# Optimization experiments

Hardware: AMD Instinct MI355X
Metric: run time of the kernel (lower is better)

The kernel has to match this reference:

```python
import jax, jax.numpy as jnp
import numpy as np

NUM_PITCHES = 128
RHYTHM_DIM = 10
HARMONY_DIM = 12
VOCAB_SIZE = 390
EPS = 1e-08


def setup_inputs() -> dict:
    key = jax.random.key(0)
    k_tok, k_w1, k_w2 = jax.random.split(key, 3)
    B, T = 1024, 8192
    stats_dim = NUM_PITCHES + RHYTHM_DIM + HARMONY_DIM  # 150
    midi_tokens = jax.random.randint(k_tok, (B, T), 0, VOCAB_SIZE, dtype=jnp.int64 if jax.config.jax_enable_x64 else jnp.int32)
    W1 = jax.random.normal(k_w1, (stats_dim, 256), dtype=jnp.float32) * 0.05
    b1 = jnp.zeros((256,), dtype=jnp.float32)
    W2 = jax.random.normal(k_w2, (256, 128), dtype=jnp.float32) * 0.05
    b2 = jnp.zeros((128,), dtype=jnp.float32)
    return {"midi_tokens": midi_tokens, "W1": W1, "b1": b1, "W2": W2, "b2": b2}


def _compute_stats(midi_tokens):
    """Vectorized pitch histogram + rhythm + harmony stats. midi_tokens: (B, T) int."""
    B, T = midi_tokens.shape
    # Pitch distribution: histogram of tokens % 128 per batch row, via one flat scatter-add.
    pitch = midi_tokens % NUM_PITCHES  # (B, T) in [0, 128)
    flat_bins = (jnp.arange(B, dtype=pitch.dtype)[:, None] * NUM_PITCHES + pitch).reshape(-1)
    hist = jnp.zeros((B * NUM_PITCHES,), dtype=jnp.float32).at[flat_bins].add(1.0)
    pitch_dist = hist.reshape(B, NUM_PITCHES)
    pitch_dist = pitch_dist / (pitch_dist.sum(axis=-1, keepdims=True) + EPS)
    # Rhythm: mean and (unbiased, torch-default) std; remaining 8 dims are zeros.
    tf = midi_tokens.astype(jnp.float32)
    mean = tf.mean(axis=-1)
    std = jnp.sqrt(((tf - mean[:, None]) ** 2).sum(axis=-1) / (T - 1))
    rhythm = jnp.zeros((B, RHYTHM_DIM), dtype=jnp.float32)
    rhythm = rhythm.at[:, 0].set(mean).at[:, 1].set(std)
    # Harmony: original uses torch.rand(12) per row; deterministic uniform here.
    harmony = jax.random.uniform(jax.random.key(42), (B, HARMONY_DIM), dtype=jnp.float32)
    return jnp.concatenate([pitch_dist, rhythm, harmony], axis=-1)  # (B, 150)


def reference(midi_tokens, W1, b1, W2, b2):
    stats = _compute_stats(midi_tokens)
    h = jax.nn.relu(stats @ W1 + b1)
    return h @ W2 + b2  # (B, feature_dim=128)
```

## Files before the change

kernel.cpp:

```cpp
#include <hip/hip_runtime.h>
#include <stdint.h>
#include <math.h>

#define T_SEQ 8192

typedef int vint4 __attribute__((ext_vector_type(4)));

__device__ __forceinline__ uint32_t rotl32(uint32_t x, int n) {
    return (x << n) | (x >> (32 - n));
}

__device__ uint32_t jax_threefry_bits_12288(uint32_t idx) {
    const uint32_t k0 = 0u, k1 = 42u, k2 = 0u ^ 42u ^ 0x1BD11BDAu;
    uint32_t i = (idx < 6144u) ? idx : (idx - 6144u);
    uint32_t x0 = i + k0;
    uint32_t x1 = (i + 6144u) + k1;
#define TF_R4(a,b,c,d) \
    x0 += x1; x1 = rotl32(x1, a); x1 ^= x0; \
    x0 += x1; x1 = rotl32(x1, b); x1 ^= x0; \
    x0 += x1; x1 = rotl32(x1, c); x1 ^= x0; \
    x0 += x1; x1 = rotl32(x1, d); x1 ^= x0;
    TF_R4(13, 15, 26, 6);   x0 += k1; x1 += k2 + 1u;
    TF_R4(17, 29, 16, 24);  x0 += k2; x1 += k0 + 2u;
    TF_R4(13, 15, 26, 6);   x0 += k0; x1 += k1 + 3u;
    TF_R4(17, 29, 16, 24);  x0 += k1; x1 += k2 + 4u;
    TF_R4(13, 15, 26, 6);   x0 += k2; x1 += k0 + 5u;
#undef TF_R4
    return (idx < 6144u) ? x0 : x1;
}

__global__ __launch_bounds__(512) void fused_kernel(const int* __restrict__ tok,
                                                    const float* __restrict__ W1,
                                                    const float* __restrict__ b1,
                                                    const float* __restrict__ W2,
                                                    const float* __restrict__ b2,
                                                    float* __restrict__ out) {
    const int tid = threadIdx.x;
    const int wave = tid >> 6;
    const int hw = tid >> 5;
    const int r0 = blockIdx.x * 2;

    __shared__ int hist[16][128];
    __shared__ int wsum[8];
    __shared__ unsigned wsq[8];
    __shared__ float s[2][150];
    __shared__ float h[2][256];
    __shared__ float part[2][128];

    for (int i = tid; i < 2048; i += 512) ((int*)hist)[i] = 0;
    __syncthreads();

    {
        const int row_local = tid >> 8;
        const int t256 = tid & 255;
        const vint4* tp = (const vint4*)(tok + (size_t)(r0 + row_local) * T_SEQ);

        vint4 v[8];
#pragma unroll
        for (int j = 0; j < 8; ++j)
            v[j] = __builtin_nontemporal_load(&tp[j * 256 + t256]);

        int sum = 0;
        unsigned sq = 0;
#pragma unroll
        for (int j = 0; j < 8; ++j) {
            atomicAdd(&hist[hw][v[j].x & 127], 1); sum += v[j].x; sq += (unsigned)__mul24(v[j].x, v[j].x);
            atomicAdd(&hist[hw][v[j].y & 127], 1); sum += v[j].y; sq += (unsigned)__mul24(v[j].y, v[j].y);
            atomicAdd(&hist[hw][v[j].z & 127], 1); sum += v[j].z; sq += (unsigned)__mul24(v[j].z, v[j].z);
            atomicAdd(&hist[hw][v[j].w & 127], 1); sum += v[j].w; sq += (unsigned)__mul24(v[j].w, v[j].w);
        }
#pragma unroll
        for (int off = 32; off > 0; off >>= 1) {
            sum += __shfl_down(sum, off);
            sq  += __shfl_down(sq, off);
        }
        if ((tid & 63) == 0) { wsum[wave] = sum; wsq[wave] = sq; }
    }
    __syncthreads();

    if (tid < 300) {
        const int r = tid >= 150;
        const int k = tid - r * 150;
        const int wb = r * 4;
        const int hb = r * 8;
        float val;
        if (k < 128) {
            int hh = (hist[hb][k] + hist[hb + 1][k]) + (hist[hb + 2][k] + hist[hb + 3][k])
                   + (hist[hb + 4][k] + hist[hb + 5][k]) + (hist[hb + 6][k] + hist[hb + 7][k]);
            val = (float)hh * (1.0f / 8192.0f);
        } else if (k == 128) {
            int ss = wsum[wb] + wsum[wb + 1] + wsum[wb + 2] + wsum[wb + 3];
            val = (float)ss * (1.0f / 8192.0f);
        } else if (k == 129) {
            double ss = (double)(wsum[wb] + wsum[wb + 1] + wsum[wb + 2] + wsum[wb + 3]);
            double qq = (double)wsq[wb] + (double)wsq[wb + 1] + (double)wsq[wb + 2] + (double)wsq[wb + 3];
            val = (float)sqrt((qq - ss * ss / 8192.0) / 8191.0);
        } else if (k < 138) {
            val = 0.0f;
        } else {
            uint32_t bits = jax_threefry_bits_12288((uint32_t)(r0 + r) * 12u + (uint32_t)(k - 138));
            val = __uint_as_float((bits >> 9) | 0x3f800000u) - 1.0f;
        }
        s[r][k] = val;
    }
    __syncthreads();

    {
        const int g = tid >> 8, c = tid & 255;
        float acc = b1[c];
#pragma unroll 5
        for (int k = 0; k < 150; ++k)
            acc = fmaf(s[g][k], W1[k * 256 + c], acc);
        h[g][c] = fmaxf(acc, 0.0f);
    }
    __syncthreads();

    {
        const int half = tid >> 8, g = (tid >> 7) & 1, c = tid & 127;
        const float* hr = h[g];
        const int kb = half * 128;
        float acc = half ? 0.0f : b2[c];
#pragma unroll 8
        for (int k = 0; k < 128; ++k)
            acc = fmaf(hr[kb + k], W2[(kb + k) * 128 + c], acc);
        if (half) part[g][c] = acc;
        __syncthreads();
        if (!half) out[(r0 + g) * 128 + c] = acc + part[g][c];
    }
}

extern "C" void kernel_launch(void* const* d_in, const int* in_sizes, int n_in,
                              void* d_out, int out_size, void* d_ws, size_t ws_size,
                              hipStream_t stream) {
    const int*   tok = (const int*)d_in[0];
    const float* W1  = (const float*)d_in[1];
    const float* b1  = (const float*)d_in[2];
    const float* W2  = (const float*)d_in[3];
    const float* b2  = (const float*)d_in[4];
    float* out = (float*)d_out;

    fused_kernel<<<512, 512, 0, stream>>>(tok, W1, b1, W2, b2, out);
}
```

Before: 98.26 us.

## Process four rows per block and share weight loads across rows in MLP

Each block now handles four rows with 1024 threads instead of two rows with 512. The MLP layers split the K dimension across thread groups, and each weight load is reused for all four rows' accumulators. Partial sums are then reduced through shared memory. This is meant to halve global weight traffic per row and cut the per-row MLP tail, in exchange for fewer blocks (256 on a GPU with many CUs), more shared memory, and an extra reduction sync.

New measurement: 98.42 us. Within noise of the previous version (+0.2%).

```diff
diff --git a/kernel.cpp b/kernel.cpp
--- a/kernel.cpp
+++ b/kernel.cpp
@@ -29,25 +29,26 @@
     return (idx < 6144u) ? x0 : x1;
 }
 
-__global__ __launch_bounds__(512) void fused_kernel(const int* __restrict__ tok,
-                                                    const float* __restrict__ W1,
-                                                    const float* __restrict__ b1,
-                                                    const float* __restrict__ W2,
-                                                    const float* __restrict__ b2,
-                                                    float* __restrict__ out) {
+__global__ __launch_bounds__(1024) void fused_kernel(const int* __restrict__ tok,
+                                                     const float* __restrict__ W1,
+                                                     const float* __restrict__ b1,
+                                                     const float* __restrict__ W2,
+                                                     const float* __restrict__ b2,
+                                                     float* __restrict__ out) {
     const int tid = threadIdx.x;
     const int wave = tid >> 6;
     const int hw = tid >> 5;
-    const int r0 = blockIdx.x * 2;
+    const int r0 = blockIdx.x * 4;
 
-    __shared__ int hist[16][128];
-    __shared__ int wsum[8];
-    __shared__ unsigned wsq[8];
-    __shared__ float s[2][150];
-    __shared__ float h[2][256];
-    __shared__ float part[2][128];
+    __shared__ int hist[32][128];
+    __shared__ int wsum[16];
+    __shared__ unsigned wsq[16];
+    __shared__ float s[4][150];
+    __shared__ float h[4][256];
+    __shared__ float part1[4][4][256];
+    __shared__ float part2[4][4][128];
 
-    for (int i = tid; i < 2048; i += 512) ((int*)hist)[i] = 0;
+    for (int i = tid; i < 4096; i += 1024) ((int*)hist)[i] = 0;
     __syncthreads();
 
     {
@@ -78,8 +79,8 @@
     }
     __syncthreads();
 
-    if (tid < 300) {
-        const int r = tid >= 150;
+    if (tid < 600) {
+        const int r = tid / 150;
         const int k = tid - r * 150;
         const int wb = r * 4;
         const int hb = r * 8;
@@ -106,26 +107,56 @@
     __syncthreads();
 
     {
-        const int g = tid >> 8, c = tid & 255;
-        float acc = b1[c];
-#pragma unroll 5
-        for (int k = 0; k < 150; ++k)
-            acc = fmaf(s[g][k], W1[k * 256 + c], acc);
-        h[g][c] = fmaxf(acc, 0.0f);
+        const int c = tid & 255;
+        const int kq = tid >> 8;
+        const int k0 = kq * 38;
+        const int k1 = (kq == 3) ? 150 : (k0 + 38);
+        float a0 = 0.0f, a1 = 0.0f, a2 = 0.0f, a3 = 0.0f;
+        for (int k = k0; k < k1; ++k) {
+            const float w = W1[k * 256 + c];
+            a0 = fmaf(s[0][k], w, a0);
+            a1 = fmaf(s[1][k], w, a1);
+            a2 = fmaf(s[2][k], w, a2);
+            a3 = fmaf(s[3][k], w, a3);
+        }
+        part1[kq][0][c] = a0;
+        part1[kq][1][c] = a1;
+        part1[kq][2][c] = a2;
+        part1[kq][3][c] = a3;
+    }
+    __syncthreads();
+    {
+        const int c = tid & 255;
+        const int r = tid >> 8;
+        float acc = b1[c] + ((part1[0][r][c] + part1[1][r][c]) + (part1[2][r][c] + part1[3][r][c]));
+        h[r][c] = fmaxf(acc, 0.0f);
     }
     __syncthreads();
 
-    {
-        const int half = tid >> 8, g = (tid >> 7) & 1, c = tid & 127;
-        const float* hr = h[g];
-        const int kb = half * 128;
-        float acc = half ? 0.0f : b2[c];
-#pragma unroll 8
-        for (int k = 0; k < 128; ++k)
-            acc = fmaf(hr[kb + k], W2[(kb + k) * 128 + c], acc);
-        if (half) part[g][c] = acc;
-        __syncthreads();
-        if (!half) out[(r0 + g) * 128 + c] = acc + part[g][c];
+    if (tid < 512) {
+        const int c = tid & 127;
+        const int kq = tid >> 7;
+        const int kb = kq * 64;
+        float a0 = 0.0f, a1 = 0.0f, a2 = 0.0f, a3 = 0.0f;
+#pragma unroll 4
+        for (int k = 0; k < 64; ++k) {
+            const float w = W2[(kb + k) * 128 + c];
+            a0 = fmaf(h[0][kb + k], w, a0);
+            a1 = fmaf(h[1][kb + k], w, a1);
+            a2 = fmaf(h[2][kb + k], w, a2);
+            a3 = fmaf(h[3][kb + k], w, a3);
+        }
+        part2[kq][0][c] = a0;
+        part2[kq][1][c] = a1;
+        part2[kq][2][c] = a2;
+        part2[kq][3][c] = a3;
+    }
+    __syncthreads();
+    if (tid < 512) {
+        const int c = tid & 127;
+        const int r = tid >> 7;
+        out[(size_t)(r0 + r) * 128 + c] =
+            b2[c] + ((part2[0][r][c] + part2[1][r][c]) + (part2[2][r][c] + part2[3][r][c]));
     }
 }
 
@@ -139,5 +170,5 @@
     const float* b2  = (const float*)d_in[4];
     float* out = (float*)d_out;
 
-    fused_kernel<<<512, 512, 0, stream>>>(tok, W1, b1, W2, b2, out);
+    fused_kernel<<<256, 1024, 0, stream>>>(tok, W1, b1, W2, b2, out);
 }
```
